# Performance work log

Hardware: AMD Instinct MI355X
Metric: run time of the kernel (lower is better)

## Reference

```python
import jax, jax.numpy as jnp
import numpy as np
from jax.ops import segment_sum, segment_max

N_M = 100000   # muon nodes
N_J = 100000   # jet nodes
E   = 1600000  # edges per relation (~avg degree 16)
D   = 64       # input feature dim
H   = 64       # hidden_channels
C   = 2        # num_classes

def setup_inputs():
    key = jax.random.key(0)
    ks = jax.random.split(key, 16)
    g = lambda k, shape, fan: jax.random.normal(k, shape, jnp.float32) / np.sqrt(fan).astype(np.float32)
    return {
        "x_muons": jax.random.normal(ks[0], (N_M, D), jnp.float32),
        "x_jets":  jax.random.normal(ks[1], (N_J, D), jnp.float32),
        "ei_mm": jax.random.randint(ks[2], (2, E), 0, N_M, jnp.int32),
        "ei_mj": jnp.stack([jax.random.randint(ks[3], (E,), 0, N_M, jnp.int32),
                            jax.random.randint(ks[4], (E,), 0, N_J, jnp.int32)]),
        "ei_jj": jax.random.randint(ks[5], (2, E), 0, N_J, jnp.int32),
        "gat_w_src": g(ks[6], (D, H), D),
        "gat_w_dst": g(ks[7], (D, H), D),
        "gat_att_src": g(ks[8], (H,), H),
        "gat_att_dst": g(ks[9], (H,), H),
        "gat_bias": jnp.zeros((H,), jnp.float32),
        "sage_w_l": g(ks[10], (D, H), D),
        "sage_w_r": g(ks[11], (D, H), D),
        "sage_bias": jnp.zeros((H,), jnp.float32),
        "gcn_w": g(ks[12], (D, H), D),
        "gcn_bias": jnp.zeros((H,), jnp.float32),
        "lin_w": g(ks[13], (H, C), H),
        "lin_b": jnp.zeros((C,), jnp.float32),
    }

def _add_self_loops(ei, n):
    loop = jnp.arange(n, dtype=ei.dtype)
    return jnp.concatenate([ei[0], loop]), jnp.concatenate([ei[1], loop])

def _gat(x, ei, w_src, w_dst, att_src, att_dst, bias):
    # PyG GATConv, heads=1, add_self_loops=True, negative_slope=0.2
    n = x.shape[0]
    src, dst = _add_self_loops(ei, n)
    hs = x @ w_src                      # [n, H] source-side messages
    hd = x @ w_dst                      # dst-side (attention only)
    a = jax.nn.leaky_relu((hs @ att_src)[src] + (hd @ att_dst)[dst], 0.2)
    m = segment_max(a, dst, num_segments=n)      # per-dst softmax (stable)
    ea = jnp.exp(a - m[dst])
    z = segment_sum(ea, dst, num_segments=n)
    alpha = ea / z[dst]                 # self loop guarantees z > 0
    return segment_sum(alpha[:, None] * hs[src], dst, num_segments=n) + bias

def _sage(x_src, x_dst, ei, w_l, w_r, bias):
    # PyG SAGEConv: mean aggregation, root weight, no self loops
    n = x_dst.shape[0]
    src, dst = ei[0], ei[1]
    agg = segment_sum(x_src[src], dst, num_segments=n)
    cnt = segment_sum(jnp.ones_like(dst, jnp.float32), dst, num_segments=n)
    mean = agg / jnp.maximum(cnt, 1.0)[:, None]
    return mean @ w_l + x_dst @ w_r + bias

def _gcn(x, ei, w, bias):
    # PyG GCNConv: symmetric gcn_norm on A + I
    n = x.shape[0]
    src, dst = _add_self_loops(ei, n)
    xw = x @ w
    deg = segment_sum(jnp.ones_like(dst, jnp.float32), dst, num_segments=n)
    dis = deg ** -0.5                   # deg >= 1 due to self loops
    norm = dis[src] * dis[dst]
    return segment_sum(norm[:, None] * xw[src], dst, num_segments=n) + bias

def reference(x_muons, x_jets, ei_mm, ei_mj, ei_jj,
              gat_w_src, gat_w_dst, gat_att_src, gat_att_dst, gat_bias,
              sage_w_l, sage_w_r, sage_bias, gcn_w, gcn_bias, lin_w, lin_b):
    # Original forward returns inside the layer loop -> exactly one HeteroConv layer runs.
    muons = _gat(x_muons, ei_mm, gat_w_src, gat_w_dst, gat_att_src, gat_att_dst, gat_bias)
    jets = (_sage(x_muons, x_jets, ei_mj, sage_w_l, sage_w_r, sage_bias)
            + _gcn(x_jets, ei_jj, gcn_w, gcn_bias))   # HeteroConv aggr='sum' on dst type 'jets'
    muons = jax.nn.relu(muons)
    jets = jax.nn.relu(jets)
    out = jnp.concatenate([muons, jets], axis=0)       # [N_M + N_J, H]
    return jax.nn.sigmoid(out @ lin_w + lin_b)
```

## Files before the change

### kernel.cpp

```cpp
#include <hip/hip_runtime.h>
#include <math.h>

#define N_M 100000
#define N_J 100000
#define NE  1600000
#define NTOT (3*N_M)
#define ETOT (3*NE)
#define NB_SCAN 293
#define DD  64
#define HH  64

#define NBIN 586
#define BIN_SHIFT 9
#define G1 640
#define EPB ((ETOT + G1 - 1) / G1)

__device__ __forceinline__ float lrelu(float a){ return fmaxf(a, 0.2f*a); }
__device__ __forceinline__ float wmax(float v){
    #pragma unroll
    for (int o = 32; o; o >>= 1) v = fmaxf(v, __shfl_xor(v, o));
    return v;
}
__device__ __forceinline__ float wsum(float v){
    #pragma unroll
    for (int o = 32; o; o >>= 1) v += __shfl_xor(v, o);
    return v;
}
__device__ __forceinline__ float sigm(float x){ return 1.f/(1.f + expf(-x)); }

__device__ __forceinline__ unsigned short f2bf(float f){
    unsigned u = __float_as_uint(f);
    u += 0x7FFFu + ((u >> 16) & 1u);
    return (unsigned short)(u >> 16);
}
__device__ __forceinline__ float bf2f(unsigned short h){
    return __uint_as_float((unsigned)h << 16);
}


__global__ void k_vdst(const float* __restrict__ w_dst, const float* __restrict__ att_dst,
                       float* __restrict__ v_dst){
    int d = threadIdx.x;
    float s = 0.f;
    for (int h = 0; h < HH; ++h) s += w_dst[d*HH + h] * att_dst[h];
    v_dst[d] = s;
}

__global__ __launch_bounds__(256) void k_muon_prep(
    const float* __restrict__ x, const float* __restrict__ w_src,
    const float* __restrict__ att_src, const float* __restrict__ v_dst,
    unsigned short* __restrict__ hs_b, float* __restrict__ as_, float* __restrict__ ad_,
    unsigned short* __restrict__ xm_b)
{
    __shared__ float lw[DD*HH];
    __shared__ float latt[HH];
    __shared__ float lvd[DD];
    int tid = threadIdx.x;
    for (int i = tid; i < DD*HH; i += 256) lw[i] = w_src[i];
    if (tid < HH) latt[tid] = att_src[tid];
    if (tid < DD) lvd[tid] = v_dst[tid];
    __syncthreads();
    int row = blockIdx.x*64 + (tid >> 2);
    int q = tid & 3;
    if (row >= N_M) return;
    const float4* x4 = (const float4*)(x + (size_t)row*DD);
    float acc[16];
    #pragma unroll
    for (int f = 0; f < 16; ++f) acc[f] = 0.f;
    float adp = 0.f;
    for (int kk = 0; kk < 16; ++kk){
        float4 xv = x4[kk];
        adp += xv.x*lvd[4*kk] + xv.y*lvd[4*kk+1] + xv.z*lvd[4*kk+2] + xv.w*lvd[4*kk+3];
        if ((kk >> 2) == q)
            *(ushort4*)(xm_b + (size_t)row*DD + 4*kk) =
                make_ushort4(f2bf(xv.x), f2bf(xv.y), f2bf(xv.z), f2bf(xv.w));
        float xs[4] = {xv.x, xv.y, xv.z, xv.w};
        #pragma unroll
        for (int j = 0; j < 4; ++j){
            const float* wp = lw + (4*kk + j)*HH + (q << 4);
            float xk = xs[j];
            #pragma unroll
            for (int f = 0; f < 16; ++f) acc[f] = fmaf(xk, wp[f], acc[f]);
        }
    }
    float asp = 0.f;
    #pragma unroll
    for (int f = 0; f < 16; ++f) asp += acc[f] * latt[(q<<4) + f];
    asp += __shfl_xor(asp, 1);
    asp += __shfl_xor(asp, 2);
    unsigned short* hp = hs_b + (size_t)row*HH + (q << 4);
    #pragma unroll
    for (int j = 0; j < 4; ++j)
        ((ushort4*)hp)[j] = make_ushort4(f2bf(acc[4*j]), f2bf(acc[4*j+1]),
                                         f2bf(acc[4*j+2]), f2bf(acc[4*j+3]));
    if (q == 0){ as_[row] = asp; ad_[row] = adp; }
}

__global__ __launch_bounds__(256) void k_gcn_xw(
    const float* __restrict__ x, const float* __restrict__ w, unsigned short* __restrict__ xw_b)
{
    __shared__ float lw[DD*HH];
    int tid = threadIdx.x;
    for (int i = tid; i < DD*HH; i += 256) lw[i] = w[i];
    __syncthreads();
    int row = blockIdx.x*64 + (tid >> 2);
    int q = tid & 3;
    if (row >= N_J) return;
    const float4* x4 = (const float4*)(x + (size_t)row*DD);
    float acc[16];
    #pragma unroll
    for (int f = 0; f < 16; ++f) acc[f] = 0.f;
    for (int kk = 0; kk < 16; ++kk){
        float4 xv = x4[kk];
        float xs[4] = {xv.x, xv.y, xv.z, xv.w};
        #pragma unroll
        for (int j = 0; j < 4; ++j){
            const float* wp = lw + (4*kk + j)*HH + (q << 4);
            float xk = xs[j];
            #pragma unroll
            for (int f = 0; f < 16; ++f) acc[f] = fmaf(xk, wp[f], acc[f]);
        }
    }
    unsigned short* hp = xw_b + (size_t)row*HH + (q << 4);
    #pragma unroll
    for (int j = 0; j < 4; ++j)
        ((ushort4*)hp)[j] = make_ushort4(f2bf(acc[4*j]), f2bf(acc[4*j+1]),
                                         f2bf(acc[4*j+2]), f2bf(acc[4*j+3]));
}

__global__ __launch_bounds__(256) void k_xr(
    const float* __restrict__ x, const float* __restrict__ w_r,
    const float* __restrict__ sb, const float* __restrict__ gb, float* __restrict__ xr)
{
    __shared__ float lw[DD*HH];
    __shared__ float lb[HH];
    int tid = threadIdx.x;
    for (int i = tid; i < DD*HH; i += 256) lw[i] = w_r[i];
    if (tid < HH) lb[tid] = sb[tid] + gb[tid];
    __syncthreads();
    int row = blockIdx.x*64 + (tid >> 2);
    int q = tid & 3;
    if (row >= N_J) return;
    const float4* x4 = (const float4*)(x + (size_t)row*DD);
    float acc[16];
    #pragma unroll
    for (int f = 0; f < 16; ++f) acc[f] = 0.f;
    for (int kk = 0; kk < 16; ++kk){
        float4 xv = x4[kk];
        float xs[4] = {xv.x, xv.y, xv.z, xv.w};
        #pragma unroll
        for (int j = 0; j < 4; ++j){
            const float* wp = lw + (4*kk + j)*HH + (q << 4);
            float xk = xs[j];
            #pragma unroll
            for (int f = 0; f < 16; ++f) acc[f] = fmaf(xk, wp[f], acc[f]);
        }
    }
    float* hp = xr + (size_t)row*HH + (q << 4);
    #pragma unroll
    for (int j = 0; j < 4; ++j){
        int f0 = (q << 4) + 4*j;
        ((float4*)hp)[j] = make_float4(acc[4*j]   + lb[f0],
                                       acc[4*j+1] + lb[f0+1],
                                       acc[4*j+2] + lb[f0+2],
                                       acc[4*j+3] + lb[f0+3]);
    }
}


__device__ __forceinline__ void edge_rd(int t, const int* ei_mm, const int* ei_mj,
                                        const int* ei_jj, const int** ei, int* r, int* e){
    if (t < NE){ *r = 0; *e = t; *ei = ei_mm; }
    else if (t < 2*NE){ *r = 1; *e = t - NE; *ei = ei_mj; }
    else { *r = 2; *e = t - 2*NE; *ei = ei_jj; }
}

__global__ __launch_bounds__(256) void k_bin0(
    const int* __restrict__ ei_mm, const int* __restrict__ ei_mj,
    const int* __restrict__ ei_jj, int* __restrict__ g_bincnt)
{
    __shared__ int bh[NBIN];
    int tid = threadIdx.x;
    for (int i = tid; i < NBIN; i += 256) bh[i] = 0;
    __syncthreads();
    int t0 = blockIdx.x * EPB;
    int t1 = min(t0 + EPB, ETOT);
    for (int t = t0 + tid; t < t1; t += 256){
        const int* ei; int r, e;
        edge_rd(t, ei_mm, ei_mj, ei_jj, &ei, &r, &e);
        int bucket = r*N_M + ei[NE + e];
        atomicAdd(&bh[bucket >> BIN_SHIFT], 1);
    }
    __syncthreads();
    for (int i = tid; i < NBIN; i += 256)
        if (bh[i]) atomicAdd(&g_bincnt[i], bh[i]);
}

__global__ void k_binscan(const int* __restrict__ g_bincnt, int* __restrict__ g_binoff,
                          int* __restrict__ g_bincur, int* __restrict__ offs)
{
    int l = threadIdx.x;
    int base = l * 10;
    int v[10]; int s = 0;
    #pragma unroll
    for (int k = 0; k < 10; ++k){
        int idx = base + k;
        v[k] = (idx < NBIN) ? g_bincnt[idx] : 0;
        s += v[k];
    }
    int inc = s;
    #pragma unroll
    for (int o = 1; o < 64; o <<= 1){
        int u = __shfl_up(inc, o);
        if (l >= o) inc += u;
    }
    int ex = inc - s;
    #pragma unroll
    for (int k = 0; k < 10; ++k){
        int idx = base + k;
        if (idx < NBIN){ g_binoff[idx] = ex; g_bincur[idx] = ex; ex += v[k]; }
    }
    if (l == 63) g_binoff[NBIN] = ex;
    if (l == 0)  offs[NTOT] = ETOT;
}

__global__ __launch_bounds__(256) void k_bin1(
    const int* __restrict__ ei_mm, const int* __restrict__ ei_mj,
    const int* __restrict__ ei_jj, int* __restrict__ g_bincur,
    unsigned* __restrict__ binned)
{
    __shared__ int bh[NBIN];
    __shared__ int cb[NBIN];
    int tid = threadIdx.x;
    for (int i = tid; i < NBIN; i += 256) bh[i] = 0;
    __syncthreads();
    int t0 = blockIdx.x * EPB;
    int t1 = min(t0 + EPB, ETOT);
    for (int t = t0 + tid; t < t1; t += 256){
        const int* ei; int r, e;
        edge_rd(t, ei_mm, ei_mj, ei_jj, &ei, &r, &e);
        int bucket = r*N_M + ei[NE + e];
        atomicAdd(&bh[bucket >> BIN_SHIFT], 1);
    }
    __syncthreads();
    for (int i = tid; i < NBIN; i += 256){
        int c = bh[i];
        cb[i] = c ? atomicAdd(&g_bincur[i], c) : 0;
        bh[i] = 0;
    }
    __syncthreads();
    for (int t = t0 + tid; t < t1; t += 256){
        const int* ei; int r, e;
        edge_rd(t, ei_mm, ei_mj, ei_jj, &ei, &r, &e);
        int s = ei[e];
        int bucket = r*N_M + ei[NE + e];
        int bin = bucket >> BIN_SHIFT;
        int lb  = bucket & 511;
        int pos = cb[bin] + atomicAdd(&bh[bin], 1);
        binned[pos] = ((unsigned)lb << 17) | (unsigned)s;
    }
}

__global__ __launch_bounds__(256) void k_build(
    const unsigned* __restrict__ binned, const int* __restrict__ g_binoff,
    int* __restrict__ offs, int* __restrict__ perm)
{
    __shared__ int lh[512];
    __shared__ int lcur[512];
    __shared__ int ls[256];
    int b = blockIdx.x, tid = threadIdx.x;
    int e0 = g_binoff[b], e1 = g_binoff[b+1];
    lh[tid] = 0; lh[tid + 256] = 0;
    __syncthreads();
    for (int e = e0 + tid; e < e1; e += 256)
        atomicAdd(&lh[binned[e] >> 17], 1);
    __syncthreads();
    int a0 = lh[2*tid], a1 = lh[2*tid + 1];
    int s = a0 + a1;
    ls[tid] = s; __syncthreads();
    for (int o = 1; o < 256; o <<= 1){
        int u = (tid >= o) ? ls[tid - o] : 0;
        __syncthreads();
        ls[tid] += u;
        __syncthreads();
    }
    int ex = ls[tid] - s;
    lcur[2*tid]     = ex;
    lcur[2*tid + 1] = ex + a0;
    int gb = b*512 + 2*tid;
    if (gb     < NTOT) offs[gb]     = e0 + ex;
    if (gb + 1 < NTOT) offs[gb + 1] = e0 + ex + a0;
    __syncthreads();
    for (int e = e0 + tid; e < e1; e += 256){
        unsigned p = binned[e];
        int pos = atomicAdd(&lcur[p >> 17], 1);
        perm[e0 + pos] = (int)(p & 0x1FFFFu);
    }
}


__global__ void k_hist(const int* __restrict__ ei_mm, const int* __restrict__ ei_mj,
                       const int* __restrict__ ei_jj, int* __restrict__ cnt){
    int t = blockIdx.x*256 + threadIdx.x;
    if (t >= ETOT) return;
    const int* ei; int r, e;
    edge_rd(t, ei_mm, ei_mj, ei_jj, &ei, &r, &e);
    atomicAdd(&cnt[r*N_M + ei[NE + e]], 1);
}

__global__ __launch_bounds__(256) void k_scan1(const int* __restrict__ cnt,
                                               int* __restrict__ offs, int* __restrict__ bsum){
    __shared__ int ls[256];
    int b = blockIdx.x, t = threadIdx.x;
    int base = b*1024 + t*4;
    int4 c = make_int4(0,0,0,0);
    if (base < NTOT) c = *(const int4*)(cnt + base);
    int s = c.x + c.y + c.z + c.w;
    ls[t] = s; __syncthreads();
    for (int o = 1; o < 256; o <<= 1){
        int a = (t >= o) ? ls[t - o] : 0;
        __syncthreads();
        ls[t] += a;
        __syncthreads();
    }
    int excl = ls[t] - s;
    if (t == 255) bsum[b] = ls[255];
    if (base < NTOT){
        offs[base]   = excl;
        offs[base+1] = excl + c.x;
        offs[base+2] = excl + c.x + c.y;
        offs[base+3] = excl + c.x + c.y + c.z;
    }
}

__global__ __launch_bounds__(512) void k_scan2(int* __restrict__ bsum){
    __shared__ int ls[512];
    int t = threadIdx.x;
    int v = (t < NB_SCAN) ? bsum[t] : 0;
    ls[t] = v; __syncthreads();
    for (int o = 1; o < 512; o <<= 1){
        int a = (t >= o) ? ls[t - o] : 0;
        __syncthreads();
        ls[t] += a;
        __syncthreads();
    }
    if (t < NB_SCAN) bsum[t] = ls[t] - v;
}

__global__ void k_scan3(int* __restrict__ offs, const int* __restrict__ bsum){
    int b = blockIdx.x, t = threadIdx.x;
    int base = b*1024 + t*4;
    if (base >= NTOT) return;
    int add = bsum[b];
    int4* p = (int4*)(offs + base);
    int4 v = *p;
    v.x += add; v.y += add; v.z += add; v.w += add;
    *p = v;
}

__global__ void k_fill(const int* __restrict__ ei_mm, const int* __restrict__ ei_mj,
                       const int* __restrict__ ei_jj, const int* __restrict__ offs,
                       int* __restrict__ cursor, int* __restrict__ perm){
    int t = blockIdx.x*256 + threadIdx.x;
    if (t >= ETOT) return;
    const int* ei; int r, e;
    edge_rd(t, ei_mm, ei_mj, ei_jj, &ei, &r, &e);
    int s = ei[e];
    int bkt = r*N_M + ei[NE + e];
    int pos = atomicAdd(&cursor[bkt], 1);
    perm[offs[bkt] + pos] = s;
}

__global__ void k_set_offs_top(int* __restrict__ offs){ offs[NTOT] = ETOT; }

__global__ void k_dis(const int* __restrict__ offs, float* __restrict__ dis){
    int j = blockIdx.x*256 + threadIdx.x;
    if (j >= N_J) return;
    int beg = offs[2*N_M + j];
    int end = (j == N_J-1) ? ETOT : offs[2*N_M + j + 1];
    dis[j] = rsqrtf((float)(end - beg + 1));
}

__global__ void k_val(const int* __restrict__ perm, const float* __restrict__ as_,
                      const float* __restrict__ dis, float* __restrict__ val){
    int t = blockIdx.x*256 + threadIdx.x;
    if (t < NE)            val[t] = as_[perm[t]];
    else if (t >= 2*NE && t < ETOT) val[t] = dis[perm[t]];
}


__global__ __launch_bounds__(512) void k_muon_gat_out(
    const int* __restrict__ offs, const int* __restrict__ perm,
    const float* __restrict__ val,
    const float* __restrict__ as_, const float* __restrict__ ad_,
    const unsigned short* __restrict__ hs_b, const float* __restrict__ gat_bias,
    const float* __restrict__ lin_w, const float* __restrict__ lin_b,
    float* __restrict__ out)
{
    int wid = threadIdx.x >> 6;
    int l = threadIdx.x & 63;
    int d = blockIdx.x*8 + wid;
    if (d >= N_M) return;
    int p = l & 15, g = l >> 4;
    int beg = offs[d], end = offs[d+1];
    float ad_d = ad_[d];
    float a_self = lrelu(as_[d] + ad_d);
    float m = a_self, z = 0.f;
    float acc0 = 0.f, acc1 = 0.f, acc2 = 0.f, acc3 = 0.f;
    for (int base = beg; base < end; base += 64){
        int e = base + l;
        int sB = 0; float aB = -1e30f;
        if (e < end){ sB = perm[e]; aB = lrelu(val[e] + ad_d); }
        float bm = wmax(aB);
        if (bm > m){
            float sc = expf(m - bm);
            acc0 *= sc; acc1 *= sc; acc2 *= sc; acc3 *= sc; z *= sc;
            m = bm;
        }
        float eaB = expf(aB - m);
        z += wsum(eaB);
        int cc = min(64, end - base);
        int k = 0;
        for (; k + 32 <= cc; k += 32){
            #pragma unroll
            for (int qq = 0; qq < 8; ++qq){
                int idx = k + qq*4 + g;
                int s = __shfl(sB, idx);
                float w = __shfl(eaB, idx);
                ushort4 v = *(const ushort4*)(hs_b + (size_t)s*HH + 4*p);
                acc0 = fmaf(w, bf2f(v.x), acc0);
                acc1 = fmaf(w, bf2f(v.y), acc1);
                acc2 = fmaf(w, bf2f(v.z), acc2);
                acc3 = fmaf(w, bf2f(v.w), acc3);
            }
        }
        for (; k < cc; k += 4){
            int idx = k + g;
            int cl = min(idx, cc - 1);
            int s = __shfl(sB, cl);
            float w = __shfl(eaB, cl);
            if (idx >= cc) w = 0.f;
            ushort4 v = *(const ushort4*)(hs_b + (size_t)s*HH + 4*p);
            acc0 = fmaf(w, bf2f(v.x), acc0);
            acc1 = fmaf(w, bf2f(v.y), acc1);
            acc2 = fmaf(w, bf2f(v.z), acc2);
            acc3 = fmaf(w, bf2f(v.w), acc3);
        }
    }
    acc0 += __shfl_xor(acc0, 16); acc0 += __shfl_xor(acc0, 32);
    acc1 += __shfl_xor(acc1, 16); acc1 += __shfl_xor(acc1, 32);
    acc2 += __shfl_xor(acc2, 16); acc2 += __shfl_xor(acc2, 32);
    acc3 += __shfl_xor(acc3, 16); acc3 += __shfl_xor(acc3, 32);
    float eself = expf(a_self - m);
    z += eself;
    ushort4 hv = *(const ushort4*)(hs_b + (size_t)d*HH + 4*p);
    acc0 = fmaf(eself, bf2f(hv.x), acc0);
    acc1 = fmaf(eself, bf2f(hv.y), acc1);
    acc2 = fmaf(eself, bf2f(hv.z), acc2);
    acc3 = fmaf(eself, bf2f(hv.w), acc3);
    float rz = 1.f / z;
    float q0 = 0.f, q1 = 0.f;
    {
        float a[4] = {acc0, acc1, acc2, acc3};
        #pragma unroll
        for (int c = 0; c < 4; ++c){
            int f = 4*p + c;
            float v2 = fmaxf(a[c]*rz + gat_bias[f], 0.f);
            q0 = fmaf(v2, lin_w[f*2 + 0], q0);
            q1 = fmaf(v2, lin_w[f*2 + 1], q1);
        }
    }
    #pragma unroll
    for (int o = 1; o <= 8; o <<= 1){ q0 += __shfl_xor(q0, o); q1 += __shfl_xor(q1, o); }
    if (l == 0){
        size_t oo = (size_t)d*2;
        out[oo]   = sigm(q0 + lin_b[0]);
        out[oo+1] = sigm(q1 + lin_b[1]);
    }
}

__global__ __launch_bounds__(512) void k_jet_out(
    const unsigned short* __restrict__ xm_b, const unsigned short* __restrict__ xw_b,
    const float* __restrict__ xr, const float* __restrict__ dis,
    const int* __restrict__ offs, const int* __restrict__ perm,
    const float* __restrict__ val, const float* __restrict__ w_l,
    const float* __restrict__ lin_w, const float* __restrict__ lin_b,
    float* __restrict__ out)
{
    __shared__ float lwl[DD*HH];
    int tid = threadIdx.x;
    for (int i = tid; i < DD*HH; i += 512) lwl[i] = w_l[i];
    __syncthreads();
    int wid = tid >> 6;
    int l = tid & 63;
    int j = blockIdx.x*8 + wid;
    if (j >= N_J) return;
    int p = l & 15, g = l >> 4;
    int beg1 = offs[N_M + j],  end1 = offs[N_M + j + 1];
    int beg2 = offs[2*N_M + j];
    int end2 = (j == N_J-1) ? ETOT : offs[2*N_M + j + 1];
    float dj = dis[j];
    float sa0 = 0.f, sa1 = 0.f, sa2 = 0.f, sa3 = 0.f;
    float gc0 = 0.f, gc1 = 0.f, gc2 = 0.f, gc3 = 0.f;
    for (int b1 = beg1, b2 = beg2; b1 < end1 || b2 < end2; b1 += 64, b2 += 64){
        int e1 = b1 + l, e2 = b2 + l;
        bool h1 = (b1 < end1), h2 = (b2 < end2);
        int sB1 = 0, sB2 = 0; float nB2 = 0.f;
        if (h1 && e1 < end1) sB1 = perm[e1];
        if (h2 && e2 < end2){ sB2 = perm[e2]; nB2 = val[e2]*dj; }
        if (h1){
            int cc = min(64, end1 - b1);
            int k = 0;
            for (; k + 16 <= cc; k += 16){
                #pragma unroll
                for (int qq = 0; qq < 4; ++qq){
                    int idx = k + qq*4 + g;
                    int s = __shfl(sB1, idx);
                    ushort4 v = *(const ushort4*)(xm_b + (size_t)s*DD + 4*p);
                    sa0 += bf2f(v.x); sa1 += bf2f(v.y); sa2 += bf2f(v.z); sa3 += bf2f(v.w);
                }
            }
            for (; k < cc; k += 4){
                int idx = k + g;
                int cl = min(idx, cc - 1);
                int s = __shfl(sB1, cl);
                float w = (idx < cc) ? 1.f : 0.f;
                ushort4 v = *(const ushort4*)(xm_b + (size_t)s*DD + 4*p);
                sa0 = fmaf(w, bf2f(v.x), sa0);
                sa1 = fmaf(w, bf2f(v.y), sa1);
                sa2 = fmaf(w, bf2f(v.z), sa2);
                sa3 = fmaf(w, bf2f(v.w), sa3);
            }
        }
        if (h2){
            int cc = min(64, end2 - b2);
            int k = 0;
            for (; k + 16 <= cc; k += 16){
                #pragma unroll
                for (int qq = 0; qq < 4; ++qq){
                    int idx = k + qq*4 + g;
                    int s = __shfl(sB2, idx);
                    float w = __shfl(nB2, idx);
                    ushort4 v = *(const ushort4*)(xw_b + (size_t)s*HH + 4*p);
                    gc0 = fmaf(w, bf2f(v.x), gc0);
                    gc1 = fmaf(w, bf2f(v.y), gc1);
                    gc2 = fmaf(w, bf2f(v.z), gc2);
                    gc3 = fmaf(w, bf2f(v.w), gc3);
                }
            }
            for (; k < cc; k += 4){
                int idx = k + g;
                int cl = min(idx, cc - 1);
                int s = __shfl(sB2, cl);
                float w = __shfl(nB2, cl);
                if (idx >= cc) w = 0.f;
                ushort4 v = *(const ushort4*)(xw_b + (size_t)s*HH + 4*p);
                gc0 = fmaf(w, bf2f(v.x), gc0);
                gc1 = fmaf(w, bf2f(v.y), gc1);
                gc2 = fmaf(w, bf2f(v.z), gc2);
                gc3 = fmaf(w, bf2f(v.w), gc3);
            }
        }
    }
    sa0 += __shfl_xor(sa0, 16); sa0 += __shfl_xor(sa0, 32);
    sa1 += __shfl_xor(sa1, 16); sa1 += __shfl_xor(sa1, 32);
    sa2 += __shfl_xor(sa2, 16); sa2 += __shfl_xor(sa2, 32);
    sa3 += __shfl_xor(sa3, 16); sa3 += __shfl_xor(sa3, 32);
    gc0 += __shfl_xor(gc0, 16); gc0 += __shfl_xor(gc0, 32);
    gc1 += __shfl_xor(gc1, 16); gc1 += __shfl_xor(gc1, 32);
    gc2 += __shfl_xor(gc2, 16); gc2 += __shfl_xor(gc2, 32);
    gc3 += __shfl_xor(gc3, 16); gc3 += __shfl_xor(gc3, 32);
    float inv = (end1 > beg1) ? 1.f/(float)(end1 - beg1) : 1.f;
    float mean_a[4] = {sa0*inv, sa1*inv, sa2*inv, sa3*inv};
    {
        ushort4 sv = *(const ushort4*)(xw_b + (size_t)j*HH + 4*p);
        float djj = dj*dj;
        gc0 = fmaf(djj, bf2f(sv.x), gc0);
        gc1 = fmaf(djj, bf2f(sv.y), gc1);
        gc2 = fmaf(djj, bf2f(sv.z), gc2);
        gc3 = fmaf(djj, bf2f(sv.w), gc3);
    }
    float b0 = __shfl(gc0, l >> 2), b1 = __shfl(gc1, l >> 2);
    float b2 = __shfl(gc2, l >> 2), b3 = __shfl(gc3, l >> 2);
    int c2 = l & 3;
    float accg_lin = (c2 == 0) ? b0 : ((c2 == 1) ? b1 : ((c2 == 2) ? b2 : b3));
    float xacc = 0.f;
    #pragma unroll
    for (int k = 0; k < 64; ++k){
        float mk = __shfl(mean_a[k & 3], k >> 2);
        xacc = fmaf(mk, lwl[k*64 + l], xacc);
    }
    float v2 = fmaxf(xacc + accg_lin + xr[(size_t)j*HH + l], 0.f);
    float q0 = wsum(v2 * lin_w[l*2 + 0]);
    float q1 = wsum(v2 * lin_w[l*2 + 1]);
    if (l == 0){
        size_t oo = (size_t)(N_M + j)*2;
        out[oo]   = sigm(q0 + lin_b[0]);
        out[oo+1] = sigm(q1 + lin_b[1]);
    }
}

extern "C" void kernel_launch(void* const* d_in, const int* in_sizes, int n_in,
                              void* d_out, int out_size, void* d_ws, size_t ws_size,
                              hipStream_t stream) {
    const float* x_muons   = (const float*)d_in[0];
    const float* x_jets    = (const float*)d_in[1];
    const int*   ei_mm     = (const int*)d_in[2];
    const int*   ei_mj     = (const int*)d_in[3];
    const int*   ei_jj     = (const int*)d_in[4];
    const float* gat_w_src = (const float*)d_in[5];
    const float* gat_w_dst = (const float*)d_in[6];
    const float* gat_att_s = (const float*)d_in[7];
    const float* gat_att_d = (const float*)d_in[8];
    const float* gat_bias  = (const float*)d_in[9];
    const float* sage_w_l  = (const float*)d_in[10];
    const float* sage_w_r  = (const float*)d_in[11];
    const float* sage_bias = (const float*)d_in[12];
    const float* gcn_w     = (const float*)d_in[13];
    const float* gcn_bias  = (const float*)d_in[14];
    const float* lin_w     = (const float*)d_in[15];
    const float* lin_b     = (const float*)d_in[16];
    float* out = (float*)d_out;

    float* ws = (float*)d_ws;
    size_t o = 0;
    unsigned short* hs_b = (unsigned short*)(ws + o); o += (size_t)N_M*HH/2;
    unsigned short* xw_b = (unsigned short*)(ws + o); o += (size_t)N_J*HH/2;
    unsigned short* xm_b = (unsigned short*)(ws + o); o += (size_t)N_M*DD/2;
    float* xr    = ws + o; o += (size_t)N_J*HH;
    float* as_   = ws + o; o += N_M;
    float* ad_   = ws + o; o += N_M;
    float* dis   = ws + o; o += N_J;
    float* v_dst = ws + o; o += 64;
    int* offs   = (int*)(ws + o); o += NTOT + 4;
    int* perm   = (int*)(ws + o); o += ETOT;
    size_t o_common = o;

    int nb64_m = (N_M + 63) / 64;
    int nb64_j = (N_J + 63) / 64;

    k_vdst<<<1, 64, 0, stream>>>(gat_w_dst, gat_att_d, v_dst);
    k_muon_prep<<<nb64_m, 256, 0, stream>>>(x_muons, gat_w_src, gat_att_s, v_dst,
                                            hs_b, as_, ad_, xm_b);
    k_gcn_xw<<<nb64_j, 256, 0, stream>>>(x_jets, gcn_w, xw_b);
    k_xr<<<nb64_j, 256, 0, stream>>>(x_jets, sage_w_r, sage_bias, gcn_bias, xr);

    float* val;
    size_t need_fast = (o_common + ETOT + 3*NBIN + 16) * sizeof(float);
    if (ws_size >= need_fast){
        unsigned* binned = (unsigned*)(ws + o); o += ETOT;
        int* g_bincnt    = (int*)(ws + o); o += NBIN;
        int* g_binoff    = (int*)(ws + o); o += NBIN + 4;
        int* g_bincur    = (int*)(ws + o); o += NBIN;
        val = (float*)binned;
        hipMemsetAsync(g_bincnt, 0, NBIN*sizeof(int), stream);
        k_bin0<<<G1, 256, 0, stream>>>(ei_mm, ei_mj, ei_jj, g_bincnt);
        k_binscan<<<1, 64, 0, stream>>>(g_bincnt, g_binoff, g_bincur, offs);
        k_bin1<<<G1, 256, 0, stream>>>(ei_mm, ei_mj, ei_jj, g_bincur, binned);
        k_build<<<NBIN, 256, 0, stream>>>(binned, g_binoff, offs, perm);
    } else {
        int* cnt    = (int*)(ws + o); o += NTOT;
        int* cursor = (int*)(ws + o); o += NTOT;
        int* bsum   = (int*)(ws + o); o += 512;
        val = ws + o; o += ETOT;
        hipMemsetAsync(cnt,    0, (size_t)NTOT*sizeof(int), stream);
        hipMemsetAsync(cursor, 0, (size_t)NTOT*sizeof(int), stream);
        int nbE3 = (ETOT + 255) / 256;
        k_hist<<<nbE3, 256, 0, stream>>>(ei_mm, ei_mj, ei_jj, cnt);
        k_scan1<<<NB_SCAN, 256, 0, stream>>>(cnt, offs, bsum);
        k_scan2<<<1, 512, 0, stream>>>(bsum);
        k_scan3<<<NB_SCAN, 256, 0, stream>>>(offs, bsum);
        k_fill<<<nbE3, 256, 0, stream>>>(ei_mm, ei_mj, ei_jj, offs, cursor, perm);
        k_set_offs_top<<<1, 1, 0, stream>>>(offs);
    }

    k_dis<<<(N_J + 255)/256, 256, 0, stream>>>(offs, dis);
    k_val<<<(ETOT + 255)/256, 256, 0, stream>>>(perm, as_, dis, val);

    k_muon_gat_out<<<(N_M + 7)/8, 512, 0, stream>>>(offs, perm, val, as_, ad_, hs_b,
                                                    gat_bias, lin_w, lin_b, out);
    k_jet_out<<<(N_J + 7)/8, 512, 0, stream>>>(xm_b, xw_b, xr, dis, offs, perm, val,
                                               sage_w_l, lin_w, lin_b, out);
}
```

Before: 441.3 us.

## Fuse jet prep GEMMs, fold v_dst and dis into kernels, drop val gather

Merges the GCN and SAGE-root jet projections into one kernel that reads x_jets once, and folds the w_dst·att_dst product into muon prep so k_vdst goes away. Degree normalisation is now computed inside k_build, which removes k_dis on the fast path. The precomputed per-edge val array is dropped, so the GAT and GCN aggregation loops now gather as_[src] and dis[src] directly. This removes three launches and one full edge pass, at the price of random gathers inside the output kernels and more register and LDS use in the fused prep kernel.

Result: no change. 449.8 us (+1.9%).

```diff
diff --git a/kernel.cpp b/kernel.cpp
--- a/kernel.cpp
+++ b/kernel.cpp
@@ -38,17 +38,10 @@
 }
 
 
-__global__ void k_vdst(const float* __restrict__ w_dst, const float* __restrict__ att_dst,
-                       float* __restrict__ v_dst){
-    int d = threadIdx.x;
-    float s = 0.f;
-    for (int h = 0; h < HH; ++h) s += w_dst[d*HH + h] * att_dst[h];
-    v_dst[d] = s;
-}
-
 __global__ __launch_bounds__(256) void k_muon_prep(
     const float* __restrict__ x, const float* __restrict__ w_src,
-    const float* __restrict__ att_src, const float* __restrict__ v_dst,
+    const float* __restrict__ w_dst, const float* __restrict__ att_src,
+    const float* __restrict__ att_dst,
     unsigned short* __restrict__ hs_b, float* __restrict__ as_, float* __restrict__ ad_,
     unsigned short* __restrict__ xm_b)
 {
@@ -58,7 +51,12 @@
     int tid = threadIdx.x;
     for (int i = tid; i < DD*HH; i += 256) lw[i] = w_src[i];
     if (tid < HH) latt[tid] = att_src[tid];
-    if (tid < DD) lvd[tid] = v_dst[tid];
+    if (tid < DD){
+        float s = 0.f;
+        #pragma unroll 8
+        for (int h = 0; h < HH; ++h) s += w_dst[tid*HH + h] * att_dst[h];
+        lvd[tid] = s;
+    }
     __syncthreads();
     int row = blockIdx.x*64 + (tid >> 2);
     int q = tid & 3;
@@ -96,74 +94,52 @@
     if (q == 0){ as_[row] = asp; ad_[row] = adp; }
 }
 
-__global__ __launch_bounds__(256) void k_gcn_xw(
-    const float* __restrict__ x, const float* __restrict__ w, unsigned short* __restrict__ xw_b)
-{
-    __shared__ float lw[DD*HH];
+__global__ __launch_bounds__(256) void k_jet_prep(
+    const float* __restrict__ x, const float* __restrict__ gcn_w,
+    const float* __restrict__ w_r, const float* __restrict__ sb,
+    const float* __restrict__ gb,
+    unsigned short* __restrict__ xw_b, float* __restrict__ xr)
+{
+    __shared__ float lwg[DD*HH];
+    __shared__ float lwr[DD*HH];
+    __shared__ float lb[HH];
     int tid = threadIdx.x;
-    for (int i = tid; i < DD*HH; i += 256) lw[i] = w[i];
+    for (int i = tid; i < DD*HH; i += 256){ lwg[i] = gcn_w[i]; lwr[i] = w_r[i]; }
+    if (tid < HH) lb[tid] = sb[tid] + gb[tid];
     __syncthreads();
     int row = blockIdx.x*64 + (tid >> 2);
     int q = tid & 3;
     if (row >= N_J) return;
     const float4* x4 = (const float4*)(x + (size_t)row*DD);
-    float acc[16];
-    #pragma unroll
-    for (int f = 0; f < 16; ++f) acc[f] = 0.f;
+    float accg[16], accr[16];
+    #pragma unroll
+    for (int f = 0; f < 16; ++f){ accg[f] = 0.f; accr[f] = 0.f; }
     for (int kk = 0; kk < 16; ++kk){
         float4 xv = x4[kk];
         float xs[4] = {xv.x, xv.y, xv.z, xv.w};
         #pragma unroll
         for (int j = 0; j < 4; ++j){
-            const float* wp = lw + (4*kk + j)*HH + (q << 4);
+            const float* wg = lwg + (4*kk + j)*HH + (q << 4);
+            const float* wr = lwr + (4*kk + j)*HH + (q << 4);
             float xk = xs[j];
             #pragma unroll
-            for (int f = 0; f < 16; ++f) acc[f] = fmaf(xk, wp[f], acc[f]);
+            for (int f = 0; f < 16; ++f){
+                accg[f] = fmaf(xk, wg[f], accg[f]);
+                accr[f] = fmaf(xk, wr[f], accr[f]);
+            }
         }
     }
     unsigned short* hp = xw_b + (size_t)row*HH + (q << 4);
-    #pragma unroll
-    for (int j = 0; j < 4; ++j)
-        ((ushort4*)hp)[j] = make_ushort4(f2bf(acc[4*j]), f2bf(acc[4*j+1]),
-                                         f2bf(acc[4*j+2]), f2bf(acc[4*j+3]));
-}
-
-__global__ __launch_bounds__(256) void k_xr(
-    const float* __restrict__ x, const float* __restrict__ w_r,
-    const float* __restrict__ sb, const float* __restrict__ gb, float* __restrict__ xr)
-{
-    __shared__ float lw[DD*HH];
-    __shared__ float lb[HH];
-    int tid = threadIdx.x;
-    for (int i = tid; i < DD*HH; i += 256) lw[i] = w_r[i];
-    if (tid < HH) lb[tid] = sb[tid] + gb[tid];
-    __syncthreads();
-    int row = blockIdx.x*64 + (tid >> 2);
-    int q = tid & 3;
-    if (row >= N_J) return;
-    const float4* x4 = (const float4*)(x + (size_t)row*DD);
-    float acc[16];
-    #pragma unroll
-    for (int f = 0; f < 16; ++f) acc[f] = 0.f;
-    for (int kk = 0; kk < 16; ++kk){
-        float4 xv = x4[kk];
-        float xs[4] = {xv.x, xv.y, xv.z, xv.w};
-        #pragma unroll
-        for (int j = 0; j < 4; ++j){
-            const float* wp = lw + (4*kk + j)*HH + (q << 4);
-            float xk = xs[j];
-            #pragma unroll
-            for (int f = 0; f < 16; ++f) acc[f] = fmaf(xk, wp[f], acc[f]);
-        }
-    }
-    float* hp = xr + (size_t)row*HH + (q << 4);
+    float* rp = xr + (size_t)row*HH + (q << 4);
     #pragma unroll
     for (int j = 0; j < 4; ++j){
+        ((ushort4*)hp)[j] = make_ushort4(f2bf(accg[4*j]), f2bf(accg[4*j+1]),
+                                         f2bf(accg[4*j+2]), f2bf(accg[4*j+3]));
         int f0 = (q << 4) + 4*j;
-        ((float4*)hp)[j] = make_float4(acc[4*j]   + lb[f0],
-                                       acc[4*j+1] + lb[f0+1],
-                                       acc[4*j+2] + lb[f0+2],
-                                       acc[4*j+3] + lb[f0+3]);
+        ((float4*)rp)[j] = make_float4(accr[4*j]   + lb[f0],
+                                       accr[4*j+1] + lb[f0+1],
+                                       accr[4*j+2] + lb[f0+2],
+                                       accr[4*j+3] + lb[f0+3]);
     }
 }
 
@@ -263,7 +239,7 @@
 
 __global__ __launch_bounds__(256) void k_build(
     const unsigned* __restrict__ binned, const int* __restrict__ g_binoff,
-    int* __restrict__ offs, int* __restrict__ perm)
+    int* __restrict__ offs, int* __restrict__ perm, float* __restrict__ dis)
 {
     __shared__ int lh[512];
     __shared__ int lcur[512];
@@ -290,6 +266,8 @@
     int gb = b*512 + 2*tid;
     if (gb     < NTOT) offs[gb]     = e0 + ex;
     if (gb + 1 < NTOT) offs[gb + 1] = e0 + ex + a0;
+    if (gb     >= 2*N_M && gb     < NTOT) dis[gb     - 2*N_M] = rsqrtf((float)a0 + 1.f);
+    if (gb + 1 >= 2*N_M && gb + 1 < NTOT) dis[gb + 1 - 2*N_M] = rsqrtf((float)a1 + 1.f);
     __syncthreads();
     for (int e = e0 + tid; e < e1; e += 256){
         unsigned p = binned[e];
@@ -381,17 +359,9 @@
     dis[j] = rsqrtf((float)(end - beg + 1));
 }
 
-__global__ void k_val(const int* __restrict__ perm, const float* __restrict__ as_,
-                      const float* __restrict__ dis, float* __restrict__ val){
-    int t = blockIdx.x*256 + threadIdx.x;
-    if (t < NE)            val[t] = as_[perm[t]];
-    else if (t >= 2*NE && t < ETOT) val[t] = dis[perm[t]];
-}
-
 
 __global__ __launch_bounds__(512) void k_muon_gat_out(
     const int* __restrict__ offs, const int* __restrict__ perm,
-    const float* __restrict__ val,
     const float* __restrict__ as_, const float* __restrict__ ad_,
     const unsigned short* __restrict__ hs_b, const float* __restrict__ gat_bias,
     const float* __restrict__ lin_w, const float* __restrict__ lin_b,
@@ -410,7 +380,7 @@
     for (int base = beg; base < end; base += 64){
         int e = base + l;
         int sB = 0; float aB = -1e30f;
-        if (e < end){ sB = perm[e]; aB = lrelu(val[e] + ad_d); }
+        if (e < end){ sB = perm[e]; aB = lrelu(as_[sB] + ad_d); }
         float bm = wmax(aB);
         if (bm > m){
             float sc = expf(m - bm);
@@ -483,7 +453,7 @@
     const unsigned short* __restrict__ xm_b, const unsigned short* __restrict__ xw_b,
     const float* __restrict__ xr, const float* __restrict__ dis,
     const int* __restrict__ offs, const int* __restrict__ perm,
-    const float* __restrict__ val, const float* __restrict__ w_l,
+    const float* __restrict__ w_l,
     const float* __restrict__ lin_w, const float* __restrict__ lin_b,
     float* __restrict__ out)
 {
@@ -507,7 +477,7 @@
         bool h1 = (b1 < end1), h2 = (b2 < end2);
         int sB1 = 0, sB2 = 0; float nB2 = 0.f;
         if (h1 && e1 < end1) sB1 = perm[e1];
-        if (h2 && e2 < end2){ sB2 = perm[e2]; nB2 = val[e2]*dj; }
+        if (h2 && e2 < end2){ sB2 = perm[e2]; nB2 = dis[sB2]*dj; }
         if (h1){
             int cc = min(64, end1 - b1);
             int k = 0;
@@ -631,7 +601,6 @@
     float* as_   = ws + o; o += N_M;
     float* ad_   = ws + o; o += N_M;
     float* dis   = ws + o; o += N_J;
-    float* v_dst = ws + o; o += 64;
     int* offs   = (int*)(ws + o); o += NTOT + 4;
     int* perm   = (int*)(ws + o); o += ETOT;
     size_t o_common = o;
@@ -639,30 +608,27 @@
     int nb64_m = (N_M + 63) / 64;
     int nb64_j = (N_J + 63) / 64;
 
-    k_vdst<<<1, 64, 0, stream>>>(gat_w_dst, gat_att_d, v_dst);
-    k_muon_prep<<<nb64_m, 256, 0, stream>>>(x_muons, gat_w_src, gat_att_s, v_dst,
+    k_muon_prep<<<nb64_m, 256, 0, stream>>>(x_muons, gat_w_src, gat_w_dst,
+                                            gat_att_s, gat_att_d,
                                             hs_b, as_, ad_, xm_b);
-    k_gcn_xw<<<nb64_j, 256, 0, stream>>>(x_jets, gcn_w, xw_b);
-    k_xr<<<nb64_j, 256, 0, stream>>>(x_jets, sage_w_r, sage_bias, gcn_bias, xr);
-
-    float* val;
+    k_jet_prep<<<nb64_j, 256, 0, stream>>>(x_jets, gcn_w, sage_w_r, sage_bias,
+                                           gcn_bias, xw_b, xr);
+
     size_t need_fast = (o_common + ETOT + 3*NBIN + 16) * sizeof(float);
     if (ws_size >= need_fast){
         unsigned* binned = (unsigned*)(ws + o); o += ETOT;
         int* g_bincnt    = (int*)(ws + o); o += NBIN;
         int* g_binoff    = (int*)(ws + o); o += NBIN + 4;
         int* g_bincur    = (int*)(ws + o); o += NBIN;
-        val = (float*)binned;
         hipMemsetAsync(g_bincnt, 0, NBIN*sizeof(int), stream);
         k_bin0<<<G1, 256, 0, stream>>>(ei_mm, ei_mj, ei_jj, g_bincnt);
         k_binscan<<<1, 64, 0, stream>>>(g_bincnt, g_binoff, g_bincur, offs);
         k_bin1<<<G1, 256, 0, stream>>>(ei_mm, ei_mj, ei_jj, g_bincur, binned);
-        k_build<<<NBIN, 256, 0, stream>>>(binned, g_binoff, offs, perm);
+        k_build<<<NBIN, 256, 0, stream>>>(binned, g_binoff, offs, perm, dis);
     } else {
         int* cnt    = (int*)(ws + o); o += NTOT;
         int* cursor = (int*)(ws + o); o += NTOT;
         int* bsum   = (int*)(ws + o); o += 512;
-        val = ws + o; o += ETOT;
         hipMemsetAsync(cnt,    0, (size_t)NTOT*sizeof(int), stream);
         hipMemsetAsync(cursor, 0, (size_t)NTOT*sizeof(int), stream);
         int nbE3 = (ETOT + 255) / 256;
@@ -672,13 +638,11 @@
         k_scan3<<<NB_SCAN, 256, 0, stream>>>(offs, bsum);
         k_fill<<<nbE3, 256, 0, stream>>>(ei_mm, ei_mj, ei_jj, offs, cursor, perm);
         k_set_offs_top<<<1, 1, 0, stream>>>(offs);
-    }
-
-    k_dis<<<(N_J + 255)/256, 256, 0, stream>>>(offs, dis);
-    k_val<<<(ETOT + 255)/256, 256, 0, stream>>>(perm, as_, dis, val);
-
-    k_muon_gat_out<<<(N_M + 7)/8, 512, 0, stream>>>(offs, perm, val, as_, ad_, hs_b,
+        k_dis<<<(N_J + 255)/256, 256, 0, stream>>>(offs, dis);
+    }
+
+    k_muon_gat_out<<<(N_M + 7)/8, 512, 0, stream>>>(offs, perm, as_, ad_, hs_b,
                                                     gat_bias, lin_w, lin_b, out);
-    k_jet_out<<<(N_J + 7)/8, 512, 0, stream>>>(xm_b, xw_b, xr, dis, offs, perm, val,
+    k_jet_out<<<(N_J + 7)/8, 512, 0, stream>>>(xm_b, xw_b, xr, dis, offs, perm,
                                                sage_w_l, lin_w, lin_b, out);
 }
```
